# Kernel optimization log

Measured on AMD Instinct MI355X. Metric: run time of the kernel, lower is better.

Reference implementation:

```python
import jax, jax.numpy as jnp
import numpy as np

FEATURE_DIM = 256
NUM_STEPS = 3
NUM_GRAPHS = 2048
ATOMS_PER_GRAPH = 64
TOTAL_ATOMS = NUM_GRAPHS * ATOMS_PER_GRAPH


def setup_inputs() -> dict:
    key = jax.random.key(0)
    k_x, k1, k2, k3, k4 = jax.random.split(key, 5)
    H = FEATURE_DIM
    s = 1.0 / np.sqrt(H)
    x = jax.random.normal(k_x, (TOTAL_ATOMS, H), dtype=jnp.float32)
    batch = jnp.repeat(jnp.arange(NUM_GRAPHS, dtype=jnp.int64), ATOMS_PER_GRAPH)
    sizes = jnp.full((NUM_GRAPHS,), ATOMS_PER_GRAPH, dtype=jnp.int64)
    # LSTM params (PyTorch layout: gates ordered i, f, g, o)
    W_ih = jax.random.uniform(k1, (4 * H, H), jnp.float32, -s, s)
    W_hh = jax.random.uniform(k2, (4 * H, H), jnp.float32, -s, s)
    b_ih = jax.random.uniform(k3, (4 * H,), jnp.float32, -s, s)
    b_hh = jax.random.uniform(k4, (4 * H,), jnp.float32, -s, s)
    return {"x": x, "batch": batch, "sizes": sizes,
            "W_ih": W_ih, "W_hh": W_hh, "b_ih": b_ih, "b_hh": b_hh}


def _lstm_cell(u, hx, cx, W_ih, W_hh, b_ih, b_hh):
    # u: input [B,H]; (hx, cx): hidden/cell [B,H]
    gates = u @ W_ih.T + b_ih + hx @ W_hh.T + b_hh  # [B, 4H]
    i, f, g, o = jnp.split(gates, 4, axis=-1)
    i, f, o = jax.nn.sigmoid(i), jax.nn.sigmoid(f), jax.nn.sigmoid(o)
    c = f * cx + i * jnp.tanh(g)
    h = o * jnp.tanh(c)
    return h, c


def _segment_softmax(scores, seg, num_segments):
    m = jax.ops.segment_max(scores, seg, num_segments=num_segments)
    e = jnp.exp(scores - m[seg])
    s = jax.ops.segment_sum(e, seg, num_segments=num_segments)
    return e / s[seg]


def reference(x, batch, sizes, W_ih, W_hh, b_ih, b_hh):
    B = sizes.shape[0]
    H = x.shape[1]
    seg = batch.astype(jnp.int32)
    h = jnp.zeros((B, H), dtype=x.dtype)
    c = jnp.zeros((B, H), dtype=x.dtype)
    q = h
    r = h
    for _ in range(NUM_STEPS):
        # torch code feeds h both as LSTM input and hidden state
        q, c = _lstm_cell(h, h, c, W_ih, W_hh, b_ih, b_hh)
        scores = jnp.sum(x * q[seg], axis=-1)              # [total_atoms]
        attn = _segment_softmax(scores, seg, B)            # per-graph softmax
        r = jax.ops.segment_sum(x * attn[:, None], seg, num_segments=B)  # [B,H]
        h = r  # torch code overwrites the LSTM hidden with r
    return jnp.concatenate([q, r], axis=-1)  # [B, 2H]
```

## Files before the change

### kernel.cpp

```cpp
#include <hip/hip_runtime.h>
#include <math.h>

#define H 256
#define NB 2048
#define APG 64

typedef __attribute__((ext_vector_type(8))) short short8;
typedef __attribute__((ext_vector_type(4))) float f32x4;

__device__ __forceinline__ unsigned short f2bf(float f) {
    unsigned u = __float_as_uint(f);
    u += 0x7fff + ((u >> 16) & 1);
    return (unsigned short)(u >> 16);
}

__global__ void prep_kernel(const float* __restrict__ W_ih, const float* __restrict__ W_hh,
                            const float* __restrict__ b_ih, const float* __restrict__ b_hh,
                            unsigned short* __restrict__ Wr, float* __restrict__ br) {
    int idx = blockIdx.x * 256 + threadIdx.x;
    int wr_row = idx >> 8, k = idx & 255;
    int hcol = wr_row >> 2, gate = wr_row & 3;
    int src = gate * 65536 + hcol * 256 + k;
    Wr[idx] = f2bf(W_ih[src] + W_hh[src]);
    if (idx < 1024) {
        int hc = idx >> 2, gt = idx & 3;
        br[idx] = b_ih[gt * 256 + hc] + b_hh[gt * 256 + hc];
    }
}

__global__ void lstm0(const float* __restrict__ br, float* __restrict__ q1,
                      float* __restrict__ c1) {
    int hc = threadIdx.x;
    float gi = br[hc * 4 + 0], gg = br[hc * 4 + 2], go = br[hc * 4 + 3];
    float si = 1.f / (1.f + __expf(-gi));
    float so = 1.f / (1.f + __expf(-go));
    float cn = si * tanhf(gg);
    c1[hc] = cn;
    q1[hc] = so * tanhf(cn);
}

__global__ __launch_bounds__(256)
void gemm_lstm(const unsigned short* __restrict__ hbf, const unsigned short* __restrict__ Wr,
               const float* __restrict__ br, float* __restrict__ c,
               float* __restrict__ qdst, int qstride) {
    __shared__ unsigned short smem[2][64 * 128];
    unsigned short* As = smem[0];
    unsigned short* Bs = smem[1];
    int t = threadIdx.x;
    int r0 = blockIdx.y * 64;
    int w0 = blockIdx.x * 64;
    int c0h = blockIdx.x * 16;
    int lane = t & 63, w = t >> 6;
    int ln = lane & 15, qd = lane >> 4;
    int m0 = w * 16;
    f32x4 acc[4] = {};
    for (int kc = 0; kc < 2; ++kc) {
        #pragma unroll
        for (int p = 0; p < 4; ++p) {
            int gid = p * 256 + t;
            int row = gid >> 4, g = gid & 15;
            int sg = g ^ (row & 15);
            *(short8*)&As[row * 128 + sg * 8] =
                *(const short8*)&hbf[(r0 + row) * H + kc * 128 + g * 8];
            *(short8*)&Bs[row * 128 + sg * 8] =
                *(const short8*)&Wr[(w0 + row) * H + kc * 128 + g * 8];
        }
        __syncthreads();
        #pragma unroll
        for (int kk = 0; kk < 4; ++kk) {
            int ga = (kk * 4 + qd) ^ ln;
            short8 a = *(short8*)&As[(m0 + ln) * 128 + ga * 8];
            #pragma unroll
            for (int t4 = 0; t4 < 4; ++t4) {
                int gb = (kk * 4 + qd) ^ ln;
                short8 b = *(short8*)&Bs[(t4 * 16 + ln) * 128 + gb * 8];
                acc[t4] = __builtin_amdgcn_mfma_f32_16x16x32_bf16(a, b, acc[t4], 0, 0, 0);
            }
        }
        __syncthreads();
    }
    float* gl = (float*)smem;
    #pragma unroll
    for (int t4 = 0; t4 < 4; ++t4)
        #pragma unroll
        for (int r = 0; r < 4; ++r)
            gl[(m0 + qd * 4 + r) * 68 + t4 * 16 + ln] = acc[t4][r];
    __syncthreads();
    #pragma unroll
    for (int p = 0; p < 4; ++p) {
        int idx = p * 256 + t;
        int row = idx >> 4, hc = idx & 15;
        float4 g4 = *(float4*)&gl[row * 68 + hc * 4];
        float4 b4 = *(const float4*)&br[(c0h + hc) * 4];
        float gi = g4.x + b4.x, gf = g4.y + b4.y, gg = g4.z + b4.z, go = g4.w + b4.w;
        float si = 1.f / (1.f + __expf(-gi));
        float sf = 1.f / (1.f + __expf(-gf));
        float so = 1.f / (1.f + __expf(-go));
        int cidx = (r0 + row) * H + c0h + hc;
        float cn = sf * c[cidx] + si * tanhf(gg);
        c[cidx] = cn;
        qdst[(r0 + row) * qstride + c0h + hc] = so * tanhf(cn);
    }
}

__global__ __launch_bounds__(256)
void attention(const float* __restrict__ x, const float* __restrict__ qsrc, int qstride,
               unsigned short* __restrict__ hbf, const float* __restrict__ c1,
               float* __restrict__ cdst, float* __restrict__ rf32, int rstride) {
    __shared__ float sc[64];
    __shared__ float pl[64];
    __shared__ float rpart[4][256];
    int g = blockIdx.x, t = threadIdx.x;
    int lane = t & 63, w = t >> 6;
    const float* xg = x + (size_t)g * APG * H;
    float4 xa[16];
    #pragma unroll
    for (int i = 0; i < 16; ++i)
        xa[i] = *(const float4*)&xg[(i * 4 + w) * H + lane * 4];
    float4 q4 = *(const float4*)&qsrc[g * qstride + lane * 4];
    if (c1) cdst[g * H + t] = c1[t];
    #pragma unroll
    for (int i = 0; i < 16; ++i) {
        float p = xa[i].x * q4.x + xa[i].y * q4.y + xa[i].z * q4.z + xa[i].w * q4.w;
        #pragma unroll
        for (int s = 32; s > 0; s >>= 1) p += __shfl_xor(p, s, 64);
        if (lane == 0) sc[i * 4 + w] = p;
    }
    __syncthreads();
    if (t < 64) {
        float s = sc[t], m = s;
        #pragma unroll
        for (int d = 32; d > 0; d >>= 1) m = fmaxf(m, __shfl_xor(m, d, 64));
        float e = __expf(s - m), sum = e;
        #pragma unroll
        for (int d = 32; d > 0; d >>= 1) sum += __shfl_xor(sum, d, 64);
        pl[t] = e / sum;
    }
    __syncthreads();
    float4 r4 = {0.f, 0.f, 0.f, 0.f};
    #pragma unroll
    for (int i = 0; i < 16; ++i) {
        float p = pl[i * 4 + w];
        r4.x += p * xa[i].x; r4.y += p * xa[i].y;
        r4.z += p * xa[i].z; r4.w += p * xa[i].w;
    }
    *(float4*)&rpart[w][lane * 4] = r4;
    __syncthreads();
    float o = rpart[0][t] + rpart[1][t] + rpart[2][t] + rpart[3][t];
    if (hbf)  hbf[g * H + t] = f2bf(o);
    if (rf32) rf32[g * rstride + t] = o;
}

extern "C" void kernel_launch(void* const* d_in, const int* in_sizes, int n_in,
                              void* d_out, int out_size, void* d_ws, size_t ws_size,
                              hipStream_t stream) {
    const float* x    = (const float*)d_in[0];
    const float* W_ih = (const float*)d_in[3];
    const float* W_hh = (const float*)d_in[4];
    const float* b_ih = (const float*)d_in[5];
    const float* b_hh = (const float*)d_in[6];
    float* out = (float*)d_out;

    char* ws = (char*)d_ws;
    unsigned short* Wr  = (unsigned short*)ws;
    float*          br  = (float*)(ws + 524288);
    unsigned short* hbf = (unsigned short*)(ws + 528384);
    float*          cbuf= (float*)(ws + 1576960);
    float*          qbuf= (float*)(ws + 3674112);
    float*          q1  = (float*)(ws + 5771264);
    float*          c1  = (float*)(ws + 5772288);

    prep_kernel<<<1024, 256, 0, stream>>>(W_ih, W_hh, b_ih, b_hh, Wr, br);
    lstm0<<<1, 256, 0, stream>>>(br, q1, c1);
    attention<<<2048, 256, 0, stream>>>(x, q1, 0, hbf, c1, cbuf, nullptr, 0);
    gemm_lstm<<<dim3(16, 32), 256, 0, stream>>>(hbf, Wr, br, cbuf, qbuf, 256);
    attention<<<2048, 256, 0, stream>>>(x, qbuf, 256, hbf, nullptr, nullptr, nullptr, 0);
    gemm_lstm<<<dim3(16, 32), 256, 0, stream>>>(hbf, Wr, br, cbuf, out, 512);
    attention<<<2048, 256, 0, stream>>>(x, out, 512, nullptr, nullptr, nullptr, out + 256, 512);
}
```

Before: 270.4 us.

## Fuse all stages into one persistent kernel with grid-wide barriers

Replaces the seven separate launches (weight prep, initial LSTM, three attention passes, two gate GEMMs) with a single persistent kernel of 512 blocks. Grid-wide atomic barriers separate the phases, and each block handles four graphs per attention phase. The aim is to remove launch gaps and the tail of each kernel. In exchange, the whole grid must be co-resident for the spin barrier to avoid deadlock, and block-level parallelism drops from 2048 to 512 in the attention phases.

```diff
diff --git a/kernel.cpp b/kernel.cpp
--- a/kernel.cpp
+++ b/kernel.cpp
@@ -2,8 +2,8 @@
 #include <math.h>
 
 #define H 256
-#define NB 2048
 #define APG 64
+#define NBLK 512
 
 typedef __attribute__((ext_vector_type(8))) short short8;
 typedef __attribute__((ext_vector_type(4))) float f32x4;
@@ -13,43 +13,83 @@
     u += 0x7fff + ((u >> 16) & 1);
     return (unsigned short)(u >> 16);
 }
-
-__global__ void prep_kernel(const float* __restrict__ W_ih, const float* __restrict__ W_hh,
-                            const float* __restrict__ b_ih, const float* __restrict__ b_hh,
-                            unsigned short* __restrict__ Wr, float* __restrict__ br) {
-    int idx = blockIdx.x * 256 + threadIdx.x;
-    int wr_row = idx >> 8, k = idx & 255;
-    int hcol = wr_row >> 2, gate = wr_row & 3;
-    int src = gate * 65536 + hcol * 256 + k;
-    Wr[idx] = f2bf(W_ih[src] + W_hh[src]);
-    if (idx < 1024) {
-        int hc = idx >> 2, gt = idx & 3;
-        br[idx] = b_ih[gt * 256 + hc] + b_hh[gt * 256 + hc];
-    }
-}
-
-__global__ void lstm0(const float* __restrict__ br, float* __restrict__ q1,
-                      float* __restrict__ c1) {
-    int hc = threadIdx.x;
-    float gi = br[hc * 4 + 0], gg = br[hc * 4 + 2], go = br[hc * 4 + 3];
-    float si = 1.f / (1.f + __expf(-gi));
-    float so = 1.f / (1.f + __expf(-go));
-    float cn = si * tanhf(gg);
-    c1[hc] = cn;
-    q1[hc] = so * tanhf(cn);
-}
-
-__global__ __launch_bounds__(256)
-void gemm_lstm(const unsigned short* __restrict__ hbf, const unsigned short* __restrict__ Wr,
-               const float* __restrict__ br, float* __restrict__ c,
-               float* __restrict__ qdst, int qstride) {
-    __shared__ unsigned short smem[2][64 * 128];
-    unsigned short* As = smem[0];
-    unsigned short* Bs = smem[1];
-    int t = threadIdx.x;
-    int r0 = blockIdx.y * 64;
-    int w0 = blockIdx.x * 64;
-    int c0h = blockIdx.x * 16;
+__device__ __forceinline__ float sigm(float v) { return 1.f / (1.f + __expf(-v)); }
+
+union SMem {
+    struct { unsigned short A[64 * 128]; unsigned short B[64 * 128]; } g;
+    float gl[64 * 68];
+    struct { float sc[64]; float pl[64]; float rpart[4][256]; } a;
+};
+
+__device__ __forceinline__ void gbar(int* cnt, int* gen) {
+    __syncthreads();
+    if (threadIdx.x == 0) {
+        __threadfence();
+        int g = __hip_atomic_load(gen, __ATOMIC_RELAXED, __HIP_MEMORY_SCOPE_AGENT);
+        int a = __hip_atomic_fetch_add(cnt, 1, __ATOMIC_ACQ_REL, __HIP_MEMORY_SCOPE_AGENT);
+        if (a == NBLK - 1) {
+            __hip_atomic_store(cnt, 0, __ATOMIC_RELAXED, __HIP_MEMORY_SCOPE_AGENT);
+            __hip_atomic_store(gen, g + 1, __ATOMIC_RELEASE, __HIP_MEMORY_SCOPE_AGENT);
+        } else {
+            while (__hip_atomic_load(gen, __ATOMIC_ACQUIRE, __HIP_MEMORY_SCOPE_AGENT) == g)
+                __builtin_amdgcn_s_sleep(2);
+        }
+        __threadfence();
+    }
+    __syncthreads();
+}
+
+__device__ __forceinline__ void attn_graph(const float* __restrict__ xg, float4 q4,
+                                           SMem* sm, int t, int lane, int w,
+                                           unsigned short* __restrict__ hout,
+                                           float* __restrict__ rout) {
+    float4 xa[16];
+    #pragma unroll
+    for (int i = 0; i < 16; ++i)
+        xa[i] = *(const float4*)&xg[(i * 4 + w) * H + lane * 4];
+    #pragma unroll
+    for (int i = 0; i < 16; ++i) {
+        float p = xa[i].x * q4.x + xa[i].y * q4.y + xa[i].z * q4.z + xa[i].w * q4.w;
+        #pragma unroll
+        for (int s = 32; s > 0; s >>= 1) p += __shfl_xor(p, s, 64);
+        if (lane == 0) sm->a.sc[i * 4 + w] = p;
+    }
+    __syncthreads();
+    if (t < 64) {
+        float s = sm->a.sc[t], m = s;
+        #pragma unroll
+        for (int d = 32; d > 0; d >>= 1) m = fmaxf(m, __shfl_xor(m, d, 64));
+        float e = __expf(s - m), sum = e;
+        #pragma unroll
+        for (int d = 32; d > 0; d >>= 1) sum += __shfl_xor(sum, d, 64);
+        sm->a.pl[t] = e / sum;
+    }
+    __syncthreads();
+    float4 r4 = {0.f, 0.f, 0.f, 0.f};
+    #pragma unroll
+    for (int i = 0; i < 16; ++i) {
+        float p = sm->a.pl[i * 4 + w];
+        r4.x += p * xa[i].x; r4.y += p * xa[i].y;
+        r4.z += p * xa[i].z; r4.w += p * xa[i].w;
+    }
+    *(float4*)&sm->a.rpart[w][lane * 4] = r4;
+    __syncthreads();
+    float o = sm->a.rpart[0][t] + sm->a.rpart[1][t] + sm->a.rpart[2][t] + sm->a.rpart[3][t];
+    if (hout) hout[t] = f2bf(o);
+    if (rout) rout[t] = o;
+    __syncthreads();
+}
+
+__device__ __forceinline__ void gemm_step(const unsigned short* __restrict__ hbf,
+                                          const unsigned short* __restrict__ Wr,
+                                          const float* __restrict__ b_ih,
+                                          const float* __restrict__ b_hh,
+                                          float* __restrict__ cbuf, int first,
+                                          float* __restrict__ qdst, int qstride,
+                                          SMem* sm, int blk, int t) {
+    int r0  = (blk >> 4) * 64;
+    int w0  = (blk & 15) * 64;
+    int c0h = (blk & 15) * 16;
     int lane = t & 63, w = t >> 6;
     int ln = lane & 15, qd = lane >> 4;
     int m0 = w * 16;
@@ -58,97 +98,116 @@
         #pragma unroll
         for (int p = 0; p < 4; ++p) {
             int gid = p * 256 + t;
-            int row = gid >> 4, g = gid & 15;
-            int sg = g ^ (row & 15);
-            *(short8*)&As[row * 128 + sg * 8] =
-                *(const short8*)&hbf[(r0 + row) * H + kc * 128 + g * 8];
-            *(short8*)&Bs[row * 128 + sg * 8] =
-                *(const short8*)&Wr[(w0 + row) * H + kc * 128 + g * 8];
+            int row = gid >> 4, gcol = gid & 15;
+            int sg = gcol ^ (row & 15);
+            *(short8*)&sm->g.A[row * 128 + sg * 8] =
+                *(const short8*)&hbf[(r0 + row) * H + kc * 128 + gcol * 8];
+            *(short8*)&sm->g.B[row * 128 + sg * 8] =
+                *(const short8*)&Wr[(w0 + row) * H + kc * 128 + gcol * 8];
         }
         __syncthreads();
         #pragma unroll
         for (int kk = 0; kk < 4; ++kk) {
             int ga = (kk * 4 + qd) ^ ln;
-            short8 a = *(short8*)&As[(m0 + ln) * 128 + ga * 8];
+            short8 a = *(short8*)&sm->g.A[(m0 + ln) * 128 + ga * 8];
             #pragma unroll
             for (int t4 = 0; t4 < 4; ++t4) {
-                int gb = (kk * 4 + qd) ^ ln;
-                short8 b = *(short8*)&Bs[(t4 * 16 + ln) * 128 + gb * 8];
-                acc[t4] = __builtin_amdgcn_mfma_f32_16x16x32_bf16(a, b, acc[t4], 0, 0, 0);
+                short8 bb = *(short8*)&sm->g.B[(t4 * 16 + ln) * 128 + ga * 8];
+                acc[t4] = __builtin_amdgcn_mfma_f32_16x16x32_bf16(a, bb, acc[t4], 0, 0, 0);
             }
         }
         __syncthreads();
     }
-    float* gl = (float*)smem;
     #pragma unroll
     for (int t4 = 0; t4 < 4; ++t4)
         #pragma unroll
         for (int r = 0; r < 4; ++r)
-            gl[(m0 + qd * 4 + r) * 68 + t4 * 16 + ln] = acc[t4][r];
+            sm->gl[(m0 + qd * 4 + r) * 68 + t4 * 16 + ln] = acc[t4][r];
     __syncthreads();
     #pragma unroll
     for (int p = 0; p < 4; ++p) {
         int idx = p * 256 + t;
         int row = idx >> 4, hc = idx & 15;
-        float4 g4 = *(float4*)&gl[row * 68 + hc * 4];
-        float4 b4 = *(const float4*)&br[(c0h + hc) * 4];
-        float gi = g4.x + b4.x, gf = g4.y + b4.y, gg = g4.z + b4.z, go = g4.w + b4.w;
-        float si = 1.f / (1.f + __expf(-gi));
-        float sf = 1.f / (1.f + __expf(-gf));
-        float so = 1.f / (1.f + __expf(-go));
-        int cidx = (r0 + row) * H + c0h + hc;
-        float cn = sf * c[cidx] + si * tanhf(gg);
-        c[cidx] = cn;
-        qdst[(r0 + row) * qstride + c0h + hc] = so * tanhf(cn);
-    }
-}
-
-__global__ __launch_bounds__(256)
-void attention(const float* __restrict__ x, const float* __restrict__ qsrc, int qstride,
-               unsigned short* __restrict__ hbf, const float* __restrict__ c1,
-               float* __restrict__ cdst, float* __restrict__ rf32, int rstride) {
-    __shared__ float sc[64];
-    __shared__ float pl[64];
-    __shared__ float rpart[4][256];
-    int g = blockIdx.x, t = threadIdx.x;
+        float4 g4 = *(float4*)&sm->gl[row * 68 + hc * 4];
+        int col = c0h + hc;
+        float bi = b_ih[col]       + b_hh[col];
+        float bg = b_ih[512 + col] + b_hh[512 + col];
+        float gi = g4.x + bi;
+        float gf = g4.y + b_ih[256 + col] + b_hh[256 + col];
+        float gg = g4.z + bg;
+        float go = g4.w + b_ih[768 + col] + b_hh[768 + col];
+        float si = sigm(gi), sf = sigm(gf), so = sigm(go);
+        int cidx = (r0 + row) * H + col;
+        float cprev = first ? (sigm(bi) * tanhf(bg)) : cbuf[cidx];
+        float cn = sf * cprev + si * tanhf(gg);
+        cbuf[cidx] = cn;
+        qdst[(r0 + row) * qstride + col] = so * tanhf(cn);
+    }
+    __syncthreads();
+}
+
+__global__ __launch_bounds__(256, 2)
+void mega(const float* __restrict__ x, const float* __restrict__ W_ih,
+          const float* __restrict__ W_hh, const float* __restrict__ b_ih,
+          const float* __restrict__ b_hh, float* __restrict__ out,
+          unsigned short* __restrict__ Wr, unsigned short* __restrict__ hbf,
+          float* __restrict__ cbuf, float* __restrict__ qbuf,
+          int* __restrict__ bar) {
+    __shared__ SMem sm;
+    int blk = blockIdx.x, t = threadIdx.x;
     int lane = t & 63, w = t >> 6;
-    const float* xg = x + (size_t)g * APG * H;
-    float4 xa[16];
-    #pragma unroll
-    for (int i = 0; i < 16; ++i)
-        xa[i] = *(const float4*)&xg[(i * 4 + w) * H + lane * 4];
-    float4 q4 = *(const float4*)&qsrc[g * qstride + lane * 4];
-    if (c1) cdst[g * H + t] = c1[t];
-    #pragma unroll
-    for (int i = 0; i < 16; ++i) {
-        float p = xa[i].x * q4.x + xa[i].y * q4.y + xa[i].z * q4.z + xa[i].w * q4.w;
-        #pragma unroll
-        for (int s = 32; s > 0; s >>= 1) p += __shfl_xor(p, s, 64);
-        if (lane == 0) sc[i * 4 + w] = p;
-    }
-    __syncthreads();
-    if (t < 64) {
-        float s = sc[t], m = s;
-        #pragma unroll
-        for (int d = 32; d > 0; d >>= 1) m = fmaxf(m, __shfl_xor(m, d, 64));
-        float e = __expf(s - m), sum = e;
-        #pragma unroll
-        for (int d = 32; d > 0; d >>= 1) sum += __shfl_xor(sum, d, 64);
-        pl[t] = e / sum;
-    }
-    __syncthreads();
-    float4 r4 = {0.f, 0.f, 0.f, 0.f};
-    #pragma unroll
-    for (int i = 0; i < 16; ++i) {
-        float p = pl[i * 4 + w];
-        r4.x += p * xa[i].x; r4.y += p * xa[i].y;
-        r4.z += p * xa[i].z; r4.w += p * xa[i].w;
-    }
-    *(float4*)&rpart[w][lane * 4] = r4;
-    __syncthreads();
-    float o = rpart[0][t] + rpart[1][t] + rpart[2][t] + rpart[3][t];
-    if (hbf)  hbf[g * H + t] = f2bf(o);
-    if (rf32) rf32[g * rstride + t] = o;
+    int* cnt = bar;
+    int* gen = bar + 16;
+
+    #pragma unroll
+    for (int rep = 0; rep < 2; ++rep) {
+        int idx = rep * 131072 + blk * 256 + t;
+        int wr_row = idx >> 8, k = idx & 255;
+        int hcol = wr_row >> 2, gate = wr_row & 3;
+        int src = gate * 65536 + hcol * 256 + k;
+        Wr[idx] = f2bf(W_ih[src] + W_hh[src]);
+    }
+
+    float4 q1;
+    {
+        float4 bi1 = *(const float4*)&b_ih[lane * 4];
+        float4 bi2 = *(const float4*)&b_hh[lane * 4];
+        float4 bg1 = *(const float4*)&b_ih[512 + lane * 4];
+        float4 bg2 = *(const float4*)&b_hh[512 + lane * 4];
+        float4 bo1 = *(const float4*)&b_ih[768 + lane * 4];
+        float4 bo2 = *(const float4*)&b_hh[768 + lane * 4];
+        q1.x = sigm(bo1.x + bo2.x) * tanhf(sigm(bi1.x + bi2.x) * tanhf(bg1.x + bg2.x));
+        q1.y = sigm(bo1.y + bo2.y) * tanhf(sigm(bi1.y + bi2.y) * tanhf(bg1.y + bg2.y));
+        q1.z = sigm(bo1.z + bo2.z) * tanhf(sigm(bi1.z + bi2.z) * tanhf(bg1.z + bg2.z));
+        q1.w = sigm(bo1.w + bo2.w) * tanhf(sigm(bi1.w + bi2.w) * tanhf(bg1.w + bg2.w));
+    }
+    __syncthreads();
+    #pragma unroll
+    for (int gi = 0; gi < 4; ++gi) {
+        int g = blk + gi * NBLK;
+        attn_graph(x + (size_t)g * APG * H, q1, &sm, t, lane, w, hbf + g * H, nullptr);
+    }
+    gbar(cnt, gen);
+
+    gemm_step(hbf, Wr, b_ih, b_hh, cbuf, 1, qbuf, 256, &sm, blk, t);
+    gbar(cnt, gen);
+    #pragma unroll
+    for (int gi = 0; gi < 4; ++gi) {
+        int g = blk + gi * NBLK;
+        float4 q4 = *(const float4*)&qbuf[g * 256 + lane * 4];
+        attn_graph(x + (size_t)g * APG * H, q4, &sm, t, lane, w, hbf + g * H, nullptr);
+    }
+    gbar(cnt, gen);
+
+    gemm_step(hbf, Wr, b_ih, b_hh, cbuf, 0, out, 512, &sm, blk, t);
+    gbar(cnt, gen);
+    #pragma unroll
+    for (int gi = 0; gi < 4; ++gi) {
+        int g = blk + gi * NBLK;
+        float4 q4 = *(const float4*)&out[g * 512 + lane * 4];
+        attn_graph(x + (size_t)g * APG * H, q4, &sm, t, lane, w, nullptr,
+                   out + g * 512 + 256);
+    }
 }
 
 extern "C" void kernel_launch(void* const* d_in, const int* in_sizes, int n_in,
@@ -162,19 +221,13 @@
     float* out = (float*)d_out;
 
     char* ws = (char*)d_ws;
-    unsigned short* Wr  = (unsigned short*)ws;
-    float*          br  = (float*)(ws + 524288);
-    unsigned short* hbf = (unsigned short*)(ws + 528384);
-    float*          cbuf= (float*)(ws + 1576960);
-    float*          qbuf= (float*)(ws + 3674112);
-    float*          q1  = (float*)(ws + 5771264);
-    float*          c1  = (float*)(ws + 5772288);
-
-    prep_kernel<<<1024, 256, 0, stream>>>(W_ih, W_hh, b_ih, b_hh, Wr, br);
-    lstm0<<<1, 256, 0, stream>>>(br, q1, c1);
-    attention<<<2048, 256, 0, stream>>>(x, q1, 0, hbf, c1, cbuf, nullptr, 0);
-    gemm_lstm<<<dim3(16, 32), 256, 0, stream>>>(hbf, Wr, br, cbuf, qbuf, 256);
-    attention<<<2048, 256, 0, stream>>>(x, qbuf, 256, hbf, nullptr, nullptr, nullptr, 0);
-    gemm_lstm<<<dim3(16, 32), 256, 0, stream>>>(hbf, Wr, br, cbuf, out, 512);
-    attention<<<2048, 256, 0, stream>>>(x, out, 512, nullptr, nullptr, nullptr, out + 256, 512);
-}
+    unsigned short* Wr   = (unsigned short*)ws;
+    unsigned short* hbf  = (unsigned short*)(ws + 524288);
+    float*          cbuf = (float*)(ws + 1572864);
+    float*          qbuf = (float*)(ws + 3670016);
+    int*            bar  = (int*)(ws + 5767168);
+
+    hipMemsetAsync(bar, 0, 256, stream);
+    mega<<<NBLK, 256, 0, stream>>>(x, W_ih, W_hh, b_ih, b_hh, out,
+                                   Wr, hbf, cbuf, qbuf, bar);
+}
```

After: 589.4 us. +118.0%, slower.
